# Performance work log

Measured on AMD Instinct MI355X. Metric: run time of the kernel, lower is better.

The kernel has to match this reference:

```python
import jax, jax.numpy as jnp
import numpy as np

N_GOAL, N_OBS, N_TASK = 16384, 65536, 8192
E1, E2 = 1048576, 1048576
B = 256            # graphs in batch
F, S = 128, 64     # dim_features, dim_state


def setup_inputs() -> dict:
    key = jax.random.key(0)
    ks = jax.random.split(key, 16)
    inp = {
        "x_goal": jax.random.normal(ks[0], (N_GOAL, F), jnp.float32),
        "x_obs": jax.random.normal(ks[1], (N_OBS, F), jnp.float32),
        "x_task": jax.random.normal(ks[2], (N_TASK, S), jnp.float32),
        "ei_go_src": jax.random.randint(ks[3], (E1,), 0, N_GOAL),
        "ei_go_dst": jax.random.randint(ks[4], (E1,), 0, N_OBS),
        "ei_ot_src": jax.random.randint(ks[5], (E2,), 0, N_OBS),
        "ei_ot_dst": jax.random.randint(ks[6], (E2,), 0, N_TASK),
        # contiguous graph assignment: 32 task nodes per graph
        "task_batch": jnp.arange(N_TASK) // (N_TASK // B),
        # GinStandardMLP (state_gin): Lin(F,S)-ReLU-Lin(S,S)-ReLU
        "W1": jax.random.normal(ks[7], (F, S), jnp.float32) * 0.05,
        "b1": jnp.zeros((S,), jnp.float32),
        "W2": jax.random.normal(ks[8], (S, S), jnp.float32) * 0.05,
        "b2": jnp.zeros((S,), jnp.float32),
        # GinUnactivatedMLP (action_gin): Lin(S,S)-ReLU-Lin(S,1)
        "W3": jax.random.normal(ks[9], (S, S), jnp.float32) * 0.05,
        "b3": jnp.zeros((S,), jnp.float32),
        "W4": jax.random.normal(ks[10], (S, 1), jnp.float32) * 0.05,
        "b4": jnp.zeros((1,), jnp.float32),
        # critic head: Lin(2,8)-ReLU-Lin(8,1)
        "Wc1": jax.random.normal(ks[11], (2, 8), jnp.float32) * 0.5,
        "bc1": jnp.zeros((8,), jnp.float32),
        "Wc2": jax.random.normal(ks[12], (8, 1), jnp.float32) * 0.5,
        "bc2": jnp.zeros((1,), jnp.float32),
    }
    return inp


def reference(x_goal, x_obs, x_task,
              ei_go_src, ei_go_dst, ei_ot_src, ei_ot_dst, task_batch,
              W1, b1, W2, b2, W3, b3, W4, b4, Wc1, bc1, Wc2, bc2):
    # --- state_gin: GINConv((goal, obs)), eps=0 ---
    agg1 = jax.ops.segment_sum(x_goal[ei_go_src], ei_go_dst, num_segments=N_OBS)
    h = x_obs + agg1                              # (1+eps)*x_dst + sum_j x_src
    h = jax.nn.relu(h @ W1 + b1)
    x1 = jax.nn.relu(h @ W2 + b2)                 # [N_OBS, S]

    # --- action_gin: GINConv((obs, task)), eps=0 ---
    agg2 = jax.ops.segment_sum(x1[ei_ot_src], ei_ot_dst, num_segments=N_TASK)
    g = x_task + agg2
    g = jax.nn.relu(g @ W3 + b3)
    x2 = g @ W4 + b4                              # [N_TASK, 1]

    # --- critic path: global max / mean pool over task nodes per graph ---
    max_pool = jax.ops.segment_max(x2, task_batch, num_segments=B)   # [B, 1]
    cnt = jax.ops.segment_sum(jnp.ones((N_TASK, 1), x2.dtype), task_batch, num_segments=B)
    mean_pool = jax.ops.segment_sum(x2, task_batch, num_segments=B) / cnt  # [B, 1]

    pooled = jnp.concatenate([max_pool.max(axis=1, keepdims=True),
                              mean_pool.mean(axis=1, keepdims=True)], axis=1)  # [B, 2]
    out = jax.nn.relu(pooled @ Wc1 + bc1) @ Wc2 + bc2                 # [B, 1]
    return out.squeeze(-1)                                            # [B]
```

## Files before the change

kernel.cpp:

```cpp
#include <hip/hip_runtime.h>
#include <hip/hip_bf16.h>


#define CAP1 2816
#define CAP2 5120
#define GEMM_BLKS 640

__global__ __launch_bounds__(256) void prep(
    const float* __restrict__ x_goal, const float* __restrict__ x_obs,
    const float* __restrict__ W, float* __restrict__ xg1,
    float* __restrict__ obs,
    const int* __restrict__ go_src, const int* __restrict__ go_dst,
    const int* __restrict__ ot_src, const int* __restrict__ ot_dst,
    int* __restrict__ gcur1, int* __restrict__ gcur2,
    int* __restrict__ pairs1, int* __restrict__ pairs2, int nblk1)
{
    __shared__ float smem[4096];
    const int tid = threadIdx.x;

    if (blockIdx.x < GEMM_BLKS) {
        float* Xs = smem;
        const float* X;
        float* O;
        int row0;
        if (blockIdx.x < 128) { X = x_goal; O = xg1; row0 = blockIdx.x * 128; }
        else                  { X = x_obs;  O = obs; row0 = (blockIdx.x - 128) * 128; }
        const int c0 = (tid & 7) * 8;
        const int trow = tid >> 3;
        const int r0 = trow * 4;
        const int swz = trow & 7;
        float acc[4][8];
        #pragma unroll
        for (int i = 0; i < 4; ++i)
            #pragma unroll
            for (int j = 0; j < 8; ++j) acc[i][j] = 0.f;

        for (int kc = 0; kc < 4; ++kc) {
            const int k0 = kc * 32;
            if (kc) __syncthreads();
            #pragma unroll
            for (int m = 0; m < 4; ++m) {
                int kb = tid & 7;
                int tr = tid >> 3;
                int row = tr * 4 + m;
                float4 v = *(const float4*)(X + (size_t)(row0 + row) * 128 + k0 + kb * 4);
                *(float4*)(Xs + row * 32 + ((kb ^ (tr & 7)) << 2)) = v;
            }
            __syncthreads();
            #pragma unroll 2
            for (int kb = 0; kb < 8; ++kb) {
                float4 xv[4];
                #pragma unroll
                for (int i = 0; i < 4; ++i)
                    xv[i] = *(const float4*)(Xs + (r0 + i) * 32 + ((kb ^ swz) << 2));
                #pragma unroll
                for (int kk = 0; kk < 4; ++kk) {
                    const float* wp = W + (size_t)(k0 + kb * 4 + kk) * 64 + c0;
                    float4 w0 = *(const float4*)(wp);
                    float4 w1 = *(const float4*)(wp + 4);
                    #pragma unroll
                    for (int i = 0; i < 4; ++i) {
                        float xk = (kk == 0) ? xv[i].x : (kk == 1) ? xv[i].y
                                 : (kk == 2) ? xv[i].z : xv[i].w;
                        acc[i][0] = fmaf(xk, w0.x, acc[i][0]);
                        acc[i][1] = fmaf(xk, w0.y, acc[i][1]);
                        acc[i][2] = fmaf(xk, w0.z, acc[i][2]);
                        acc[i][3] = fmaf(xk, w0.w, acc[i][3]);
                        acc[i][4] = fmaf(xk, w1.x, acc[i][4]);
                        acc[i][5] = fmaf(xk, w1.y, acc[i][5]);
                        acc[i][6] = fmaf(xk, w1.z, acc[i][6]);
                        acc[i][7] = fmaf(xk, w1.w, acc[i][7]);
                    }
                }
            }
        }
        #pragma unroll
        for (int i = 0; i < 4; ++i) {
            float4 o0; o0.x = acc[i][0]; o0.y = acc[i][1]; o0.z = acc[i][2]; o0.w = acc[i][3];
            float4 o1; o1.x = acc[i][4]; o1.y = acc[i][5]; o1.z = acc[i][6]; o1.w = acc[i][7];
            float* p = O + (size_t)(row0 + r0 + i) * 64 + c0;
            *(float4*)p = o0;
            *(float4*)(p + 4) = o1;
        }
    } else {
        int* hist = (int*)smem;
        int* cur  = (int*)smem + 512;
        const int blk2 = blockIdx.x - GEMM_BLKS;
        const bool s1 = blk2 < nblk1;
        const int* src = s1 ? go_src : ot_src;
        const int* dst = s1 ? go_dst : ot_dst;
        int* gcur  = s1 ? gcur1 : gcur2;
        int* pairs = s1 ? pairs1 : pairs2;
        const int bsh  = s1 ? 7 : 5;
        const int rowm = s1 ? 127 : 31;
        const int nb   = s1 ? 512 : 256;
        const int cap  = s1 ? CAP1 : CAP2;
        const int blk  = s1 ? blk2 : blk2 - nblk1;

        for (int i = tid; i < nb; i += 256) hist[i] = 0;
        __syncthreads();
        const int base = blk * 4096;
        const int4* d4 = (const int4*)(dst + base);
        const int4* s4 = (const int4*)(src + base);
        int4 dv[4];
        #pragma unroll
        for (int k = 0; k < 4; ++k) {
            dv[k] = d4[k * 256 + tid];
            atomicAdd(&hist[dv[k].x >> bsh], 1);
            atomicAdd(&hist[dv[k].y >> bsh], 1);
            atomicAdd(&hist[dv[k].z >> bsh], 1);
            atomicAdd(&hist[dv[k].w >> bsh], 1);
        }
        __syncthreads();
        for (int i = tid; i < nb; i += 256)
            cur[i] = atomicAdd(&gcur[i], hist[i]);
        __syncthreads();
        #pragma unroll
        for (int k = 0; k < 4; ++k) {
            int4 sv = s4[k * 256 + tid];
            int d, s, b, p;
            d = dv[k].x; s = sv.x; b = d >> bsh; p = atomicAdd(&cur[b], 1);
            if (p < cap) pairs[(size_t)b * cap + p] = ((d & rowm) << 17) | s;
            d = dv[k].y; s = sv.y; b = d >> bsh; p = atomicAdd(&cur[b], 1);
            if (p < cap) pairs[(size_t)b * cap + p] = ((d & rowm) << 17) | s;
            d = dv[k].z; s = sv.z; b = d >> bsh; p = atomicAdd(&cur[b], 1);
            if (p < cap) pairs[(size_t)b * cap + p] = ((d & rowm) << 17) | s;
            d = dv[k].w; s = sv.w; b = d >> bsh; p = atomicAdd(&cur[b], 1);
            if (p < cap) pairs[(size_t)b * cap + p] = ((d & rowm) << 17) | s;
        }
    }
}

__global__ __launch_bounds__(1024) void gather_mlp_obs(
    const int* __restrict__ pairs, const int* __restrict__ cnt,
    const float* __restrict__ xg1, const float* __restrict__ obs,
    const float* __restrict__ b1, const float* __restrict__ W2,
    const float* __restrict__ b2, float* __restrict__ x1)
{
    constexpr int ROWS = 128;
    __shared__ int ssrc[CAP1];
    __shared__ int offs[ROWS + 1];
    __shared__ int rcnt[ROWS];
    __shared__ float W2t[64 * 68];
    __shared__ float hb[16 * 64];
    const int tid = threadIdx.x;
    const int b = blockIdx.x;

    #pragma unroll
    for (int i = tid; i < 4096; i += 1024) {
        int k = i >> 6, c = i & 63;
        W2t[c * 68 + k] = W2[i];
    }
    if (tid < ROWS) rcnt[tid] = 0;
    __syncthreads();
    int n = cnt[b];
    if (n > CAP1) n = CAP1;
    const int* bp = pairs + (size_t)b * CAP1;

    int e0 = -1, e1 = -1, e2 = -1;
    {
        int i = tid;
        if (i < n) {
            e0 = bp[i]; atomicAdd(&rcnt[e0 >> 17], 1); i += 1024;
            if (i < n) {
                e1 = bp[i]; atomicAdd(&rcnt[e1 >> 17], 1); i += 1024;
                if (i < n) { e2 = bp[i]; atomicAdd(&rcnt[e2 >> 17], 1); }
            }
        }
    }
    __syncthreads();
    if (tid < 64) {
        int v0 = rcnt[2 * tid], v1 = rcnt[2 * tid + 1];
        int s = v0 + v1;
        #pragma unroll
        for (int d = 1; d < 64; d <<= 1) {
            int t = __shfl_up(s, d);
            if (tid >= d) s += t;
        }
        int ex = s - v0 - v1;
        offs[2 * tid] = ex;
        offs[2 * tid + 1] = ex + v0;
        rcnt[2 * tid] = ex;
        rcnt[2 * tid + 1] = ex + v0;
        if (tid == 63) offs[ROWS] = s;
    }
    __syncthreads();
    if (e0 >= 0) { int p = atomicAdd(&rcnt[e0 >> 17], 1); ssrc[p] = e0 & 0x1FFFF; }
    if (e1 >= 0) { int p = atomicAdd(&rcnt[e1 >> 17], 1); ssrc[p] = e1 & 0x1FFFF; }
    if (e2 >= 0) { int p = atomicAdd(&rcnt[e2 >> 17], 1); ssrc[p] = e2 & 0x1FFFF; }
    __syncthreads();
    const int wv = tid >> 6;
    const int lane = tid & 63;
    const float bb1 = b1[lane];
    const float bb2 = b2[lane];
    float* hp = hb + wv * 64;
    const float4* h4 = (const float4*)hp;
    const float4* wrow = (const float4*)(W2t + lane * 68);
    for (int r = wv; r < ROWS; r += 16) {
        int beg = offs[r], end = offs[r + 1];
        float a0 = 0.f, a1 = 0.f, a2 = 0.f, a3 = 0.f;
        int e = beg;
        for (; e + 4 <= end; e += 4) {
            int s0 = ssrc[e], s1 = ssrc[e + 1], s2 = ssrc[e + 2], s3 = ssrc[e + 3];
            a0 += xg1[(size_t)s0 * 64 + lane];
            a1 += xg1[(size_t)s1 * 64 + lane];
            a2 += xg1[(size_t)s2 * 64 + lane];
            a3 += xg1[(size_t)s3 * 64 + lane];
        }
        for (; e < end; ++e)
            a0 += xg1[(size_t)ssrc[e] * 64 + lane];
        size_t gi = (((size_t)b * ROWS) + r) * 64 + lane;
        float acc = (a0 + a1) + (a2 + a3) + obs[gi];
        hp[lane] = fmaxf(acc + bb1, 0.f);
        float a = bb2;
        #pragma unroll 8
        for (int kc = 0; kc < 16; ++kc) {
            float4 hv = h4[kc];
            float4 wv4 = wrow[kc];
            a = fmaf(hv.x, wv4.x, a);
            a = fmaf(hv.y, wv4.y, a);
            a = fmaf(hv.z, wv4.z, a);
            a = fmaf(hv.w, wv4.w, a);
        }
        x1[gi] = fmaxf(a, 0.f);
    }
}

__global__ __launch_bounds__(1024) void gather_mlp_task_pool(
    const int* __restrict__ pairs, const int* __restrict__ cnt,
    const float* __restrict__ x1, const float* __restrict__ x_task,
    const float* __restrict__ W3, const float* __restrict__ b3,
    const float* __restrict__ W4, const float* __restrict__ b4,
    const float* __restrict__ Wc1, const float* __restrict__ bc1,
    const float* __restrict__ Wc2, const float* __restrict__ bc2,
    float* __restrict__ out)
{
    constexpr int ROWS = 32;
    __shared__ int ssrc[CAP2];
    __shared__ int offs[ROWS + 1];
    __shared__ int rcnt[ROWS];
    __shared__ float W3t[64 * 68];
    __shared__ float hb[16 * 64];
    __shared__ float xrow[ROWS];
    const int tid = threadIdx.x;
    const int b = blockIdx.x;

    #pragma unroll
    for (int i = tid; i < 4096; i += 1024) {
        int k = i >> 6, c = i & 63;
        W3t[c * 68 + k] = W3[i];
    }
    if (tid < ROWS) rcnt[tid] = 0;
    __syncthreads();
    int n = cnt[b];
    if (n > CAP2) n = CAP2;
    const int* bp = pairs + (size_t)b * CAP2;

    int e0 = -1, e1 = -1, e2 = -1, e3 = -1, e4 = -1;
    {
        int i = tid;
        if (i < n) { e0 = bp[i]; atomicAdd(&rcnt[e0 >> 17], 1); i += 1024;
        if (i < n) { e1 = bp[i]; atomicAdd(&rcnt[e1 >> 17], 1); i += 1024;
        if (i < n) { e2 = bp[i]; atomicAdd(&rcnt[e2 >> 17], 1); i += 1024;
        if (i < n) { e3 = bp[i]; atomicAdd(&rcnt[e3 >> 17], 1); i += 1024;
        if (i < n) { e4 = bp[i]; atomicAdd(&rcnt[e4 >> 17], 1); } } } } }
    }
    __syncthreads();
    if (tid < 32) {
        int v = rcnt[tid];
        int s = v;
        #pragma unroll
        for (int d = 1; d < 32; d <<= 1) {
            int t = __shfl_up(s, d);
            if (tid >= d) s += t;
        }
        int ex = s - v;
        offs[tid] = ex;
        rcnt[tid] = ex;
        if (tid == 31) offs[ROWS] = s;
    }
    __syncthreads();
    if (e0 >= 0) { int p = atomicAdd(&rcnt[e0 >> 17], 1); ssrc[p] = e0 & 0x1FFFF; }
    if (e1 >= 0) { int p = atomicAdd(&rcnt[e1 >> 17], 1); ssrc[p] = e1 & 0x1FFFF; }
    if (e2 >= 0) { int p = atomicAdd(&rcnt[e2 >> 17], 1); ssrc[p] = e2 & 0x1FFFF; }
    if (e3 >= 0) { int p = atomicAdd(&rcnt[e3 >> 17], 1); ssrc[p] = e3 & 0x1FFFF; }
    if (e4 >= 0) { int p = atomicAdd(&rcnt[e4 >> 17], 1); ssrc[p] = e4 & 0x1FFFF; }
    __syncthreads();

    const int wv = tid >> 6;
    const int lane = tid & 63;
    const float bb3 = b3[lane];
    const float w4l = W4[lane];
    const float b4c = b4[0];
    float* hp = hb + wv * 64;
    const float4* h4 = (const float4*)hp;
    const float4* wrow = (const float4*)(W3t + lane * 68);
    #pragma unroll
    for (int half = 0; half < 2; ++half) {
        const int r = wv + half * 16;
        const int row = b * ROWS + r;
        int beg = offs[r], end = offs[r + 1];
        float a0 = 0.f, a1 = 0.f, a2 = 0.f, a3 = 0.f;
        float a4 = 0.f, a5 = 0.f, a6 = 0.f, a7 = 0.f;
        int e = beg;
        for (; e + 8 <= end; e += 8) {
            int s0 = ssrc[e],     s1 = ssrc[e + 1], s2 = ssrc[e + 2], s3 = ssrc[e + 3];
            int s4 = ssrc[e + 4], s5 = ssrc[e + 5], s6 = ssrc[e + 6], s7 = ssrc[e + 7];
            a0 += x1[(size_t)s0 * 64 + lane];
            a1 += x1[(size_t)s1 * 64 + lane];
            a2 += x1[(size_t)s2 * 64 + lane];
            a3 += x1[(size_t)s3 * 64 + lane];
            a4 += x1[(size_t)s4 * 64 + lane];
            a5 += x1[(size_t)s5 * 64 + lane];
            a6 += x1[(size_t)s6 * 64 + lane];
            a7 += x1[(size_t)s7 * 64 + lane];
        }
        for (; e < end; ++e)
            a0 += x1[(size_t)ssrc[e] * 64 + lane];
        float t = ((a0 + a1) + (a2 + a3)) + ((a4 + a5) + (a6 + a7))
                + x_task[(size_t)row * 64 + lane];
        hp[lane] = t;
        float a = bb3;
        #pragma unroll 8
        for (int kc = 0; kc < 16; ++kc) {
            float4 hv = h4[kc];
            float4 wv4 = wrow[kc];
            a = fmaf(hv.x, wv4.x, a);
            a = fmaf(hv.y, wv4.y, a);
            a = fmaf(hv.z, wv4.z, a);
            a = fmaf(hv.w, wv4.w, a);
        }
        float p = fmaxf(a, 0.f) * w4l;
        p += __shfl_xor(p, 1);
        p += __shfl_xor(p, 2);
        p += __shfl_xor(p, 4);
        p += __shfl_xor(p, 8);
        p += __shfl_xor(p, 16);
        p += __shfl_xor(p, 32);
        if (lane == 0) xrow[r] = p + b4c;
    }
    __syncthreads();
    if (tid == 0) {
        float mx = -1e30f, sm = 0.f;
        #pragma unroll
        for (int i = 0; i < ROWS; ++i) {
            float v = xrow[i];
            mx = fmaxf(mx, v);
            sm += v;
        }
        float mn = sm * (1.f / 32.f);
        float o = bc2[0];
        #pragma unroll
        for (int j = 0; j < 8; ++j) {
            float t = fmaxf(mx * Wc1[j] + mn * Wc1[8 + j] + bc1[j], 0.f);
            o = fmaf(t, Wc2[j], o);
        }
        out[b] = o;
    }
}

extern "C" void kernel_launch(void* const* d_in, const int* in_sizes, int n_in,
                              void* d_out, int out_size, void* d_ws, size_t ws_size,
                              hipStream_t stream)
{
    const float* x_goal = (const float*)d_in[0];
    const float* x_obs  = (const float*)d_in[1];
    const float* x_task = (const float*)d_in[2];
    const int* go_src = (const int*)d_in[3];
    const int* go_dst = (const int*)d_in[4];
    const int* ot_src = (const int*)d_in[5];
    const int* ot_dst = (const int*)d_in[6];
    const float* W1  = (const float*)d_in[8];
    const float* b1  = (const float*)d_in[9];
    const float* W2  = (const float*)d_in[10];
    const float* b2  = (const float*)d_in[11];
    const float* W3  = (const float*)d_in[12];
    const float* b3  = (const float*)d_in[13];
    const float* W4  = (const float*)d_in[14];
    const float* b4  = (const float*)d_in[15];
    const float* Wc1 = (const float*)d_in[16];
    const float* bc1 = (const float*)d_in[17];
    const float* Wc2 = (const float*)d_in[18];
    const float* bc2 = (const float*)d_in[19];
    float* out = (float*)d_out;

    const int N_OBS = 65536, N_GOAL = 16384;
    const int E1 = in_sizes[3], E2 = in_sizes[5];
    const int NB1 = 512, NB2 = 256;

    char* w = (char*)d_ws;
    float* obs    = (float*)w;  w += (size_t)N_OBS * 64 * 4;
    float* x1     = (float*)w;  w += (size_t)N_OBS * 64 * 4;
    float* xg1    = (float*)w;  w += (size_t)N_GOAL * 64 * 4;
    int*   pairs1 = (int*)w;    w += (size_t)NB1 * CAP1 * 4;
    int*   pairs2 = (int*)w;    w += (size_t)NB2 * CAP2 * 4;
    int*   gcur1  = (int*)w;    w += NB1 * 4;
    int*   gcur2  = (int*)w;    w += NB2 * 4;

    hipMemsetAsync(gcur1, 0, (NB1 + NB2) * 4, stream);

    const int nblk1 = E1 / 4096;
    const int nblk2 = E2 / 4096;
    prep<<<GEMM_BLKS + nblk1 + nblk2, 256, 0, stream>>>(
        x_goal, x_obs, W1, xg1, obs,
        go_src, go_dst, ot_src, ot_dst, gcur1, gcur2, pairs1, pairs2, nblk1);
    gather_mlp_obs<<<NB1, 1024, 0, stream>>>(pairs1, gcur1, xg1, obs, b1, W2, b2, x1);
    gather_mlp_task_pool<<<NB2, 1024, 0, stream>>>(pairs2, gcur2, x1, x_task,
                                                   W3, b3, W4, b4,
                                                   Wc1, bc1, Wc2, bc2, out);
}
```

Before: 234.0 us.

## Double-buffer GEMM X tiles with direct global-to-LDS async loads

Replaces the register-staged global-to-shared copy of the X tile in the prep GEMM with __builtin_amdgcn_global_load_lds, which writes directly into LDS. LDS is now two buffers, so the next k-chunk loads while the current one is computed. The aim is to hide global load latency and drop register round-trips. The cost is doubled shared memory per block, which may lower occupancy. Correctness also depends on the swizzled address mapping matching the reader and on the barrier waiting for the async loads to finish.

```diff
diff --git a/kernel.cpp b/kernel.cpp
--- a/kernel.cpp
+++ b/kernel.cpp
@@ -15,11 +15,10 @@
     int* __restrict__ gcur1, int* __restrict__ gcur2,
     int* __restrict__ pairs1, int* __restrict__ pairs2, int nblk1)
 {
-    __shared__ float smem[4096];
+    __shared__ float smem[8192];
     const int tid = threadIdx.x;
 
     if (blockIdx.x < GEMM_BLKS) {
-        float* Xs = smem;
         const float* X;
         float* O;
         int row0;
@@ -29,30 +28,48 @@
         const int trow = tid >> 3;
         const int r0 = trow * 4;
         const int swz = trow & 7;
+        const int w = tid >> 6;
+        const int lane = tid & 63;
+        const int srow = w * 32 + (lane >> 3);
+        const int skbx = lane & 7;
+
         float acc[4][8];
         #pragma unroll
         for (int i = 0; i < 4; ++i)
             #pragma unroll
             for (int j = 0; j < 8; ++j) acc[i][j] = 0.f;
 
+        float* bufA = smem;
+        float* bufB = smem + 4096;
+
+        auto stage = [&](float* buf, int k0) {
+            #pragma unroll
+            for (int m = 0; m < 4; ++m) {
+                int row = srow + m * 8;
+                int kg = skbx ^ ((row >> 2) & 7);
+                const float* gp = X + (size_t)(row0 + row) * 128 + k0 + kg * 4;
+                __builtin_amdgcn_global_load_lds(
+                    (const __attribute__((address_space(1))) unsigned int*)gp,
+                    (__attribute__((address_space(3))) unsigned int*)
+                        (buf + (w * 4 + m) * 256),
+                    16, 0, 0);
+            }
+        };
+
+        stage(bufA, 0);
+        __syncthreads();
+
+        float* cur = bufA;
+        float* nxt = bufB;
         for (int kc = 0; kc < 4; ++kc) {
             const int k0 = kc * 32;
-            if (kc) __syncthreads();
-            #pragma unroll
-            for (int m = 0; m < 4; ++m) {
-                int kb = tid & 7;
-                int tr = tid >> 3;
-                int row = tr * 4 + m;
-                float4 v = *(const float4*)(X + (size_t)(row0 + row) * 128 + k0 + kb * 4);
-                *(float4*)(Xs + row * 32 + ((kb ^ (tr & 7)) << 2)) = v;
-            }
-            __syncthreads();
+            if (kc < 3) stage(nxt, k0 + 32);
             #pragma unroll 2
             for (int kb = 0; kb < 8; ++kb) {
                 float4 xv[4];
                 #pragma unroll
                 for (int i = 0; i < 4; ++i)
-                    xv[i] = *(const float4*)(Xs + (r0 + i) * 32 + ((kb ^ swz) << 2));
+                    xv[i] = *(const float4*)(cur + (r0 + i) * 32 + ((kb ^ swz) << 2));
                 #pragma unroll
                 for (int kk = 0; kk < 4; ++kk) {
                     const float* wp = W + (size_t)(k0 + kb * 4 + kk) * 64 + c0;
@@ -73,6 +90,8 @@
                     }
                 }
             }
+            __syncthreads();
+            float* t = cur; cur = nxt; nxt = t;
         }
         #pragma unroll
         for (int i = 0; i < 4; ++i) {
```

New measurement: 232.6 us. About the same (-0.6%).
